# Kernel tuning notes

Measured on AMD Instinct MI355X. Metric: run time of the kernel, lower is better.

Reference implementation:

```python
import jax, jax.numpy as jnp
import numpy as np

B, S, L, E, H, T, V, D = 32, 256, 24, 300, 256, 16, 50000, 256  # batch, sents, words/sent, emb, gru_units, topics, vocab, dense


def setup_inputs() -> dict:
    key = jax.random.key(0)
    ks = jax.random.split(key, 12)
    word_ids = jax.random.randint(ks[0], (B, S, L), 0, V, dtype=jnp.int32)
    tsize = S // T
    starts = (jnp.arange(T, dtype=jnp.int32) * tsize + 1)          # 1-indexed inclusive
    ends = (jnp.arange(T, dtype=jnp.int32) * tsize + tsize)
    topic_start_ends = jnp.broadcast_to(jnp.stack([starts, ends], -1)[None], (B, T, 2))
    g = lambda k, shape, sc=0.05: (jax.random.normal(k, shape, jnp.float32) * sc)
    return {
        "word_ids": word_ids,
        "topic_start_ends": topic_start_ends,
        "emb": g(ks[1], (V, E), 0.1),
        "Wih_f": g(ks[2], (3 * H, E)), "Whh_f": g(ks[3], (3 * H, H)),
        "bih_f": jnp.zeros((3 * H,), jnp.float32), "bhh_f": jnp.zeros((3 * H,), jnp.float32),
        "Wih_b": g(ks[4], (3 * H, E)), "Whh_b": g(ks[5], (3 * H, H)),
        "bih_b": jnp.zeros((3 * H,), jnp.float32), "bhh_b": jnp.zeros((3 * H,), jnp.float32),
        "W_att": g(ks[6], (4 * H, 4 * H)), "v_att": g(ks[7], (4 * H, 1)),
        "W_dna": g(ks[8], (4 * H, D)), "b_dna": jnp.zeros((D,), jnp.float32),
        "W_out": g(ks[9], (D, 1)), "b_out": jnp.zeros((1,), jnp.float32),
    }


def _gru_dir(x, Wih, Whh, bih, bhh, reverse):
    # x: [B, S, E] -> outputs [B, S, H], final hidden [B, H]  (PyTorch GRU cell math)
    def step(h, xt):
        gi = xt @ Wih.T + bih
        gh = h @ Whh.T + bhh
        ir, iz, inn = jnp.split(gi, 3, axis=-1)
        hr, hz, hn = jnp.split(gh, 3, axis=-1)
        r = jax.nn.sigmoid(ir + hr)
        z = jax.nn.sigmoid(iz + hz)
        n = jnp.tanh(inn + r * hn)
        h2 = (1.0 - z) * n + z * h
        return h2, h2
    h0 = jnp.zeros((x.shape[0], Whh.shape[1]), x.dtype)
    hT, ys = jax.lax.scan(step, h0, jnp.swapaxes(x, 0, 1), reverse=reverse)
    return jnp.swapaxes(ys, 0, 1), hT


def _gather_seq(x, idx):
    # x: [B, S', C], idx: [B, K] -> [B, K, C]
    return jnp.take_along_axis(x, idx[:, :, None].astype(jnp.int32), axis=1)


def reference(word_ids, topic_start_ends, emb, Wih_f, Whh_f, bih_f, bhh_f,
              Wih_b, Whh_b, bih_b, bhh_b, W_att, v_att, W_dna, b_dna, W_out, b_out):
    # --- sent_encoder: per-sentence mean of word embeddings ---
    sent_vecs = jnp.mean(emb[word_ids], axis=2)  # [B, S, E]

    # --- doc_encoder: bidirectional GRU ---
    out_f, hT_f = _gru_dir(sent_vecs, Wih_f, Whh_f, bih_f, bhh_f, reverse=False)
    out_b, hT_b = _gru_dir(sent_vecs, Wih_b, Whh_b, bih_b, bhh_b, reverse=True)
    sent_rep = jnp.concatenate([out_f, out_b], axis=-1)          # [B, S, 2H]
    hidden = jnp.stack([hT_f, hT_b], axis=0)                     # [2, B, H]
    # faithful to torch: hidden.view(batch_size, 2H) (row-major reshape)
    doc_vec = hidden.reshape(B, 2 * H)
    doc_rep = jnp.broadcast_to(doc_vec[:, None, :], (B, S, 2 * H))

    # --- topic representation via boundary differencing on front/back-padded output ---
    padded = jnp.pad(sent_rep, ((0, 0), (1, 1), (0, 0)))         # [B, S+2, 2H]
    starts = topic_start_ends[..., 0]                            # [B, T], 1-indexed
    ends = topic_start_ends[..., 1]
    topic_fwd = _gather_seq(padded, ends)[..., :H] - _gather_seq(padded, starts - 1)[..., :H]
    topic_bwd = _gather_seq(padded, starts)[..., H:] - _gather_seq(padded, ends + 1)[..., H:]
    topic_mat = jnp.concatenate([topic_fwd, topic_bwd], axis=-1)  # [B, T, 2H]
    # sentence s (0-indexed) -> topic t with starts[t] <= s+1 <= ends[t]
    sent_1idx = jnp.arange(1, S + 1, dtype=jnp.int32)
    topic_id = jax.vmap(lambda e: jnp.searchsorted(e, sent_1idx, side='left'))(ends)  # [B, S]
    topic_rep = jnp.take_along_axis(topic_mat, topic_id[:, :, None], axis=1)          # [B, S, 2H]

    # --- decoder_attention ---
    cat_ds = jnp.concatenate([doc_rep, sent_rep], axis=-1)       # [B, S, 4H]
    cat_ts = jnp.concatenate([topic_rep, sent_rep], axis=-1)
    doc_scores = jnp.tanh(cat_ds @ W_att) @ v_att                # [B, S, 1]
    topic_scores = jnp.tanh(cat_ts @ W_att) @ v_att
    doc_w = jax.nn.softmax(doc_scores, axis=1)
    topic_w = jax.nn.softmax(topic_scores, axis=1)
    context = doc_w * doc_rep + topic_w * topic_rep              # [B, S, 2H]
    inp = jnp.concatenate([sent_rep, context], axis=-1)          # [B, S, 4H]
    h = jax.nn.relu(inp @ W_dna + b_dna)                         # dropout is identity (eval)
    logits = (h @ W_out + b_out)[..., 0]                         # [B, S]
    return logits
```

## Files before the change

kernel.cpp:

```cpp
#include <hip/hip_runtime.h>
#include <hip/hip_bf16.h>
#include <math.h>

#define Bd 32
#define Sd 256
#define Ld 24
#define Ed 300
#define Hd 256
#define Td 16
#define Dd 256
#define EP 320

using short8 = __attribute__((ext_vector_type(8))) short;
using f32x4  = __attribute__((ext_vector_type(4))) float;

__device__ __forceinline__ float fsigm(float x) { return 1.f / (1.f + __expf(-x)); }
__device__ __forceinline__ float ftanh(float x) {
  float e = __expf(2.f * x);
  return 1.f - 2.f / (e + 1.f);
}

__global__ void sentprep_kernel(const int* __restrict__ wids,
                                const float* __restrict__ emb,
                                __hip_bfloat16* __restrict__ apad,
                                const float* __restrict__ wih_f, const float* __restrict__ wih_b,
                                const float* __restrict__ whh_f, const float* __restrict__ whh_b,
                                __hip_bfloat16* __restrict__ wpadf, __hip_bfloat16* __restrict__ wpadb,
                                __hip_bfloat16* __restrict__ whhbf_f, __hip_bfloat16* __restrict__ whhbf_b,
                                const float* __restrict__ bih_f, const float* __restrict__ bih_b,
                                float* __restrict__ bias_cat) {
  const int blk = blockIdx.x;
  const int tid = threadIdx.x;
  if (blk < 8192) {
    __shared__ int ids[Ld];
    if (tid < Ld) ids[tid] = wids[blk * Ld + tid];
    __syncthreads();
    float acc = 0.f;
    if (tid < Ed) {
#pragma unroll
      for (int w = 0; w < Ld; ++w) acc += emb[(size_t)ids[w] * Ed + tid];
      acc *= (1.f / 24.f);
    }
    apad[blk * EP + tid] = __float2bfloat16(tid < Ed ? acc : 0.f);
    return;
  }
  const int i = (blk - 8192) * 320 + tid;
  const int PW = 768 * EP;
  const int WH = 768 * Hd;
  if (i < 2 * PW) {
    const float* src = (i < PW) ? wih_f : wih_b;
    __hip_bfloat16* dst = (i < PW) ? wpadf : wpadb;
    int j = (i < PW) ? i : i - PW;
    int n = j / EP, k = j % EP;
    dst[j] = __float2bfloat16(k < Ed ? src[n * Ed + k] : 0.f);
  } else if (i < 2 * PW + 2 * WH) {
    int j = i - 2 * PW;
    const float* src = (j < WH) ? whh_f : whh_b;
    __hip_bfloat16* dst = (j < WH) ? whhbf_f : whhbf_b;
    int k = (j < WH) ? j : j - WH;
    dst[k] = __float2bfloat16(src[k]);
  } else if (i < 2 * PW + 2 * WH + 1536) {
    int j = i - 2 * PW - 2 * WH;
    bias_cat[j] = (j < 768) ? bih_f[j] : bih_b[j - 768];
  }
}

__global__ __launch_bounds__(256) void gemm_gi_kernel(
    const __hip_bfloat16* __restrict__ A,
    const __hip_bfloat16* __restrict__ W,
    float* __restrict__ gif, float* __restrict__ gib,
    const float* __restrict__ bias_cat) {
  __shared__ unsigned short la[128][40];
  __shared__ unsigned short lb[128][40];
  const int tid = threadIdx.x;
  const int m0 = blockIdx.x * 128, n0 = blockIdx.y * 128;
  const int lane = tid & 63, wid = tid >> 6;
  const int wm = (wid >> 1) * 64, wn = (wid & 1) * 64;
  const int lrow = tid >> 2, lcol = (tid & 3) * 8;
  const int fr = lane & 15, fq = (lane >> 4) * 8;
  f32x4 acc[4][4];
#pragma unroll
  for (int i = 0; i < 4; ++i)
#pragma unroll
    for (int j = 0; j < 4; ++j) acc[i][j] = (f32x4){0.f, 0.f, 0.f, 0.f};

  for (int k0 = 0; k0 < EP; k0 += 32) {
    uint4 a0 = *(const uint4*)(A + (size_t)(m0 + lrow) * EP + k0 + lcol);
    uint4 a1 = *(const uint4*)(A + (size_t)(m0 + 64 + lrow) * EP + k0 + lcol);
    uint4 b0 = *(const uint4*)(W + (size_t)(n0 + lrow) * EP + k0 + lcol);
    uint4 b1 = *(const uint4*)(W + (size_t)(n0 + 64 + lrow) * EP + k0 + lcol);
    *(uint4*)(&la[lrow][lcol]) = a0;
    *(uint4*)(&la[64 + lrow][lcol]) = a1;
    *(uint4*)(&lb[lrow][lcol]) = b0;
    *(uint4*)(&lb[64 + lrow][lcol]) = b1;
    __syncthreads();
    short8 af[4], bf[4];
#pragma unroll
    for (int i = 0; i < 4; ++i) af[i] = *(const short8*)(&la[wm + i * 16 + fr][fq]);
#pragma unroll
    for (int j = 0; j < 4; ++j) bf[j] = *(const short8*)(&lb[wn + j * 16 + fr][fq]);
#pragma unroll
    for (int i = 0; i < 4; ++i)
#pragma unroll
      for (int j = 0; j < 4; ++j)
        acc[i][j] = __builtin_amdgcn_mfma_f32_16x16x32_bf16(af[i], bf[j], acc[i][j], 0, 0, 0);
    __syncthreads();
  }
  const int rq = (lane >> 4) * 4;
#pragma unroll
  for (int i = 0; i < 4; ++i)
#pragma unroll
    for (int j = 0; j < 4; ++j) {
      int n = n0 + wn + j * 16 + fr;
      float bv = bias_cat[n];
      float* Cp = (n < 768) ? gif : gib;
      int nn = (n < 768) ? n : n - 768;
#pragma unroll
      for (int r2 = 0; r2 < 4; ++r2) {
        int m = m0 + wm + i * 16 + rq + r2;
        Cp[(size_t)m * 768 + nn] = acc[i][j][r2] + bv;
      }
    }
}

__global__ __launch_bounds__(256) void gemm3_kernel(
    const __hip_bfloat16* __restrict__ srepbf, const __hip_bfloat16* __restrict__ topbf,
    const __hip_bfloat16* __restrict__ dvbf,
    const __hip_bfloat16* __restrict__ wpack1, const __hip_bfloat16* __restrict__ wpack2,
    float* __restrict__ QU, float* __restrict__ RT, float* __restrict__ PD) {
  const int blk = blockIdx.x;
  const __hip_bfloat16* A; const __hip_bfloat16* W; float* C;
  int M, m0, n0;
  if (blk < 640) {
    A = srepbf; W = wpack2; C = QU; M = 8192;
    m0 = (blk & 63) * 128; n0 = (blk >> 6) * 128;
  } else if (blk < 680) {
    int x = blk - 640;
    A = topbf; W = wpack1; C = RT; M = 512;
    m0 = (x & 3) * 128; n0 = (x >> 2) * 128;
  } else {
    int x = blk - 680;
    A = dvbf; W = wpack1; C = PD; M = 32;
    m0 = 0; n0 = x * 128;
  }
  __shared__ unsigned short la[128][40];
  __shared__ unsigned short lb[128][40];
  const int tid = threadIdx.x;
  const int lane = tid & 63, wid = tid >> 6;
  const int wm = (wid >> 1) * 64, wn = (wid & 1) * 64;
  const int lrow = tid >> 2, lcol = (tid & 3) * 8;
  const int fr = lane & 15, fq = (lane >> 4) * 8;
  int ar0 = m0 + lrow;      if (ar0 > M - 1) ar0 = M - 1;
  int ar1 = m0 + 64 + lrow; if (ar1 > M - 1) ar1 = M - 1;
  f32x4 acc[4][4];
#pragma unroll
  for (int i = 0; i < 4; ++i)
#pragma unroll
    for (int j = 0; j < 4; ++j) acc[i][j] = (f32x4){0.f, 0.f, 0.f, 0.f};

  for (int k0 = 0; k0 < 512; k0 += 32) {
    uint4 a0 = *(const uint4*)(A + (size_t)ar0 * 512 + k0 + lcol);
    uint4 a1 = *(const uint4*)(A + (size_t)ar1 * 512 + k0 + lcol);
    uint4 b0 = *(const uint4*)(W + (size_t)(n0 + lrow) * 512 + k0 + lcol);
    uint4 b1 = *(const uint4*)(W + (size_t)(n0 + 64 + lrow) * 512 + k0 + lcol);
    *(uint4*)(&la[lrow][lcol]) = a0;
    *(uint4*)(&la[64 + lrow][lcol]) = a1;
    *(uint4*)(&lb[lrow][lcol]) = b0;
    *(uint4*)(&lb[64 + lrow][lcol]) = b1;
    __syncthreads();
    short8 af[4], bf[4];
#pragma unroll
    for (int i = 0; i < 4; ++i) af[i] = *(const short8*)(&la[wm + i * 16 + fr][fq]);
#pragma unroll
    for (int j = 0; j < 4; ++j) bf[j] = *(const short8*)(&lb[wn + j * 16 + fr][fq]);
#pragma unroll
    for (int i = 0; i < 4; ++i)
#pragma unroll
      for (int j = 0; j < 4; ++j)
        acc[i][j] = __builtin_amdgcn_mfma_f32_16x16x32_bf16(af[i], bf[j], acc[i][j], 0, 0, 0);
    __syncthreads();
  }
  const int rq = (lane >> 4) * 4;
#pragma unroll
  for (int i = 0; i < 4; ++i)
#pragma unroll
    for (int j = 0; j < 4; ++j) {
      int n = n0 + wn + j * 16 + fr;
#pragma unroll
      for (int r2 = 0; r2 < 4; ++r2) {
        int m = m0 + wm + i * 16 + rq + r2;
        if (m < M) C[(size_t)m * 1280 + n] = acc[i][j][r2];
      }
    }
}

__global__ __launch_bounds__(512, 1) void gru_mfma_kernel(
    const float* __restrict__ gi_f, const float* __restrict__ gi_b,
    const __hip_bfloat16* __restrict__ whhbf_f, const __hip_bfloat16* __restrict__ whhbf_b,
    const float* __restrict__ bhh_f, const float* __restrict__ bhh_b,
    float* __restrict__ sent_rep, __hip_bfloat16* __restrict__ sent_rep_bf,
    float* __restrict__ hT_f, float* __restrict__ hT_b,
    const float* __restrict__ w_att, const float* __restrict__ w_dna,
    __hip_bfloat16* __restrict__ wpack1, __hip_bfloat16* __restrict__ wpack2) {
  __shared__ float gi_lds[2][8][768];
  __shared__ __hip_bfloat16 h_bf[2][256];
  __shared__ float gh[768];
  __shared__ float stg32[2][8][256];
  const int blk = blockIdx.x;
  const int tid = threadIdx.x;

  if (blk >= 64) {
    const size_t q = (size_t)(blk - 64) * 512 + tid;
    size_t flat = q * 8;
    const size_t HALF = (size_t)1280 * 512;
    const bool second = flat >= HALF;
    size_t r = second ? flat - HALF : flat;
    int n = (int)(r >> 9), k0 = (int)(r & 511);
    __hip_bfloat16* dst = second ? wpack2 : wpack1;
#pragma unroll
    for (int j = 0; j < 8; ++j) {
      int k = k0 + j;
      float v;
      if (!second)
        v = (n < 1024) ? w_att[(size_t)k * 1024 + n]
                       : w_dna[(size_t)(512 + k) * 256 + (n - 1024)];
      else
        v = (n < 1024) ? w_att[(size_t)(512 + k) * 1024 + n]
                       : w_dna[(size_t)k * 256 + (n - 1024)];
      dst[(size_t)n * 512 + k] = __float2bfloat16(v);
    }
    return;
  }

  const int dir = blk >> 5, b = blk & 31;
  const int lane = tid & 63, w = tid >> 6;
  const float* gi = dir ? gi_b : gi_f;
  const __hip_bfloat16* whh = dir ? whhbf_b : whhbf_f;
  const float* bhh = dir ? bhh_b : bhh_f;

  {
#pragma unroll
    for (int i = 0; i < 3; ++i) {
      int idx = tid + i * 512;
      int u = idx / 192;
      int c4 = (idx - u * 192) * 4;
      int s = dir ? (255 - u) : u;
      const float* g = gi + (size_t)(((b << 8) + s) * 768 + c4);
      __builtin_amdgcn_global_load_lds(
          (const __attribute__((address_space(1))) unsigned int*)g,
          (__attribute__((address_space(3))) unsigned int*)&gi_lds[0][u][c4], 16, 0, 0);
    }
  }
  if (tid < 256) h_bf[0][tid] = __float2bfloat16(0.f);

  const int fr = lane & 15, kq = (lane >> 4) * 8;
  short8 bfrag[6][8];
  {
    const int n0 = w * 96 + fr;
#pragma unroll
    for (int nt = 0; nt < 6; ++nt)
#pragma unroll
      for (int kt = 0; kt < 8; ++kt)
        bfrag[nt][kt] = *(const short8*)(whh + (size_t)(n0 + nt * 16) * 256 + kt * 32 + kq);
  }

  float bhr = 0.f, bhz = 0.f, bhn = 0.f, hprev = 0.f;
  if (tid < 256) { bhr = bhh[tid]; bhz = bhh[256 + tid]; bhn = bhh[512 + tid]; }

  asm volatile("s_waitcnt vmcnt(0) lgkmcnt(0)\n\ts_barrier" ::: "memory");

  for (int t = 0; t < Sd; ++t) {
    const int rb = t & 1, wb = rb ^ 1;

    float gl0 = 0.f, gl1 = 0.f, gl2 = 0.f;
    if (tid < 256) {
      const float* gl = gi_lds[(t >> 3) & 1][t & 7];
      gl0 = gl[tid]; gl1 = gl[256 + tid]; gl2 = gl[512 + tid];
    }

    f32x4 acc[6];
#pragma unroll
    for (int nt = 0; nt < 6; ++nt) acc[nt] = (f32x4){0.f, 0.f, 0.f, 0.f};
#pragma unroll
    for (int kt = 0; kt < 8; ++kt) {
      short8 av = *(const short8*)(&h_bf[rb][kt * 32 + kq]);
#pragma unroll
      for (int nt = 0; nt < 6; ++nt)
        acc[nt] = __builtin_amdgcn_mfma_f32_16x16x32_bf16(av, bfrag[nt][kt], acc[nt], 0, 0, 0);
      __builtin_amdgcn_sched_group_barrier(0x100, 1, 0);
      __builtin_amdgcn_sched_group_barrier(0x008, 6, 0);
    }
    if (lane < 16) {
#pragma unroll
      for (int nt = 0; nt < 6; ++nt) gh[w * 96 + nt * 16 + lane] = acc[nt][0];
    }
    asm volatile("s_waitcnt lgkmcnt(0)\n\ts_barrier" ::: "memory");

    if (tid < 256) {
      float rr = fsigm(gl0 + gh[tid] + bhr);
      float zz = fsigm(gl1 + gh[256 + tid] + bhz);
      float nn = ftanh(gl2 + rr * (gh[512 + tid] + bhn));
      float hn = (1.f - zz) * nn + zz * hprev;
      hprev = hn;
      h_bf[wb][tid] = __float2bfloat16(hn);
      stg32[(t >> 3) & 1][t & 7][tid] = hn;
    } else if ((t & 7) == 0) {
      if (t + 8 < Sd) {
        const int buf = ((t >> 3) + 1) & 1;
#pragma unroll
        for (int i = 0; i < 6; ++i) {
          int idx = (tid - 256) + i * 256;
          int u = idx / 192;
          int c4 = (idx - u * 192) * 4;
          int s = dir ? (255 - (t + 8 + u)) : (t + 8 + u);
          const float* g = gi + (size_t)(((b << 8) + s) * 768 + c4);
          __builtin_amdgcn_global_load_lds(
              (const __attribute__((address_space(1))) unsigned int*)g,
              (__attribute__((address_space(3))) unsigned int*)&gi_lds[buf][u][c4], 16, 0, 0);
        }
      }
      if (t >= 8) {
        const int base = t - 8;
        const int gp = ((t >> 3) - 1) & 1;
        const int d = tid - 256;
#pragma unroll
        for (int u = 0; u < 8; ++u) {
          int sg = dir ? (255 - (base + u)) : (base + u);
          size_t rowg = (size_t)((b << 8) + sg);
          int col = dir ? (256 + d) : d;
          float v = stg32[gp][u][d];
          sent_rep[rowg * 512 + col] = v;
          sent_rep_bf[rowg * 512 + col] = __float2bfloat16(v);
        }
      }
    }
    if (w >= 4 && (t & 7) == 7)
      asm volatile("s_waitcnt vmcnt(0)" ::: "memory");
    asm volatile("s_waitcnt lgkmcnt(0)\n\ts_barrier" ::: "memory");
  }

  if (w >= 4) {
    const int base = 248, d = tid - 256;
#pragma unroll
    for (int u = 0; u < 8; ++u) {
      int sg = dir ? (255 - (base + u)) : (base + u);
      size_t rowg = (size_t)((b << 8) + sg);
      int col = dir ? (256 + d) : d;
      float v = stg32[1][u][d];
      sent_rep[rowg * 512 + col] = v;
      sent_rep_bf[rowg * 512 + col] = __float2bfloat16(v);
    }
  } else {
    (dir ? hT_b : hT_f)[b * 256 + tid] = hprev;
  }
}

__global__ void dt_kernel(const int* __restrict__ tse, const float* __restrict__ sent_rep,
                          const float* __restrict__ hTf, const float* __restrict__ hTb,
                          __hip_bfloat16* __restrict__ topic_bf, __hip_bfloat16* __restrict__ dv) {
  const int blk = blockIdx.x;
  const int tid = threadIdx.x;
  if (blk < 512) {
    int bt = blk;
    int b = bt >> 4;
    int st = tse[bt * 2], en = tse[bt * 2 + 1];
    auto pad = [&](int i, int col) -> float {
      if (i < 1 || i > Sd) return 0.f;
      return sent_rep[((size_t)((b << 8) + (i - 1))) * 512 + col];
    };
    float fwd = pad(en, tid) - pad(st - 1, tid);
    float bwd = pad(st, Hd + tid) - pad(en + 1, Hd + tid);
    topic_bf[(size_t)bt * 512 + tid] = __float2bfloat16(fwd);
    topic_bf[(size_t)bt * 512 + Hd + tid] = __float2bfloat16(bwd);
    return;
  }
  const int b = blk - 512;
#pragma unroll
  for (int r = 0; r < 2; ++r) {
    int jj = tid + r * 256;
    int idx = b * 512 + jj;
    int dsel = idx >> 13;
    int rem = idx & 8191;
    int bp = rem >> 8, hp = rem & 255;
    float v = (dsel ? hTb : hTf)[bp * Hd + hp];
    dv[idx] = __float2bfloat16(v);
  }
}

__global__ void scores_kernel(const float* __restrict__ PD, const float* __restrict__ RT,
                              const float* __restrict__ QU, const float* __restrict__ v_att,
                              const int* __restrict__ tse,
                              float* __restrict__ dsc, float* __restrict__ tsc) {
  int r = blockIdx.x;
  int b = r >> 8, s = r & 255;
  int tid = threadIdx.x;
  int tsel = Td - 1;
  for (int t = 0; t < Td; ++t) {
    if (tse[(b * Td + t) * 2 + 1] >= s + 1) { tsel = t; break; }
  }
  const float* q = QU + (size_t)r * 1280;
  const float* p = PD + (size_t)b * 1280;
  const float* rr = RT + (size_t)(b * Td + tsel) * 1280;
  float accd = 0.f, acct = 0.f;
  for (int n = tid; n < 1024; n += 256) {
    float qv = q[n];
    float vv = v_att[n];
    accd += ftanh(p[n] + qv) * vv;
    acct += ftanh(rr[n] + qv) * vv;
  }
  __shared__ float s1[256], s2[256];
  s1[tid] = accd; s2[tid] = acct;
  __syncthreads();
  for (int off = 128; off > 0; off >>= 1) {
    if (tid < off) { s1[tid] += s1[tid + off]; s2[tid] += s2[tid + off]; }
    __syncthreads();
  }
  if (tid == 0) { dsc[r] = s1[0]; tsc[r] = s2[0]; }
}

__global__ void softmax_kernel(const float* __restrict__ dsc, const float* __restrict__ tsc,
                               float* __restrict__ dw, float* __restrict__ tw) {
  int b = blockIdx.x, s = threadIdx.x;
  __shared__ float red[256];
  for (int which = 0; which < 2; ++which) {
    const float* src = which ? tsc : dsc;
    float v = src[b * Sd + s];
    red[s] = v; __syncthreads();
    for (int off = 128; off > 0; off >>= 1) {
      if (s < off) red[s] = fmaxf(red[s], red[s + off]);
      __syncthreads();
    }
    float m = red[0]; __syncthreads();
    float e = __expf(v - m);
    red[s] = e; __syncthreads();
    for (int off = 128; off > 0; off >>= 1) {
      if (s < off) red[s] += red[s + off];
      __syncthreads();
    }
    float sum = red[0]; __syncthreads();
    (which ? tw : dw)[b * Sd + s] = e / sum;
  }
}

__global__ void final_kernel(const float* __restrict__ QU, const float* __restrict__ PD,
                             const float* __restrict__ RT, const float* __restrict__ dw,
                             const float* __restrict__ tw, const float* __restrict__ b_dna,
                             const float* __restrict__ w_out,
                             const float* __restrict__ b_out,
                             const int* __restrict__ tse, float* __restrict__ out) {
  int r = blockIdx.x;
  int b = r >> 8, s = r & 255;
  int dd = threadIdx.x;
  int tsel = Td - 1;
  for (int t = 0; t < Td; ++t) {
    if (tse[(b * Td + t) * 2 + 1] >= s + 1) { tsel = t; break; }
  }
  float wdv = dw[b * Sd + s], wtv = tw[b * Sd + s];
  float x = QU[(size_t)r * 1280 + 1024 + dd] + wdv * PD[(size_t)b * 1280 + 1024 + dd] +
            wtv * RT[(size_t)(b * Td + tsel) * 1280 + 1024 + dd] + b_dna[dd];
  x = fmaxf(x, 0.f);
  float term = x * w_out[dd];
  __shared__ float red[256];
  red[dd] = term; __syncthreads();
  for (int off = 128; off > 0; off >>= 1) {
    if (dd < off) red[dd] += red[dd + off];
    __syncthreads();
  }
  if (dd == 0) out[r] = red[0] + b_out[0];
}

extern "C" void kernel_launch(void* const* d_in, const int* in_sizes, int n_in,
                              void* d_out, int out_size, void* d_ws, size_t ws_size,
                              hipStream_t stream) {
  const int* word_ids = (const int*)d_in[0];
  const int* tse      = (const int*)d_in[1];
  const float* emb   = (const float*)d_in[2];
  const float* wih_f = (const float*)d_in[3];
  const float* whh_f = (const float*)d_in[4];
  const float* bih_f = (const float*)d_in[5];
  const float* bhh_f = (const float*)d_in[6];
  const float* wih_b = (const float*)d_in[7];
  const float* whh_b = (const float*)d_in[8];
  const float* bih_b = (const float*)d_in[9];
  const float* bhh_b = (const float*)d_in[10];
  const float* w_att = (const float*)d_in[11];
  const float* v_att = (const float*)d_in[12];
  const float* w_dna = (const float*)d_in[13];
  const float* b_dna = (const float*)d_in[14];
  const float* w_out = (const float*)d_in[15];
  const float* b_out = (const float*)d_in[16];
  float* out = (float*)d_out;
  char* ws = (char*)d_ws;

  const int M = Bd * Sd;

  size_t off = 0;
  auto alloc = [&](size_t sz) { size_t o = off; off += (sz + 255) & ~(size_t)255; return o; };
  size_t o_svbf   = alloc((size_t)M * EP * 2);
  size_t o_wpad   = alloc((size_t)2 * 768 * EP * 2);
  size_t o_whhbf  = alloc((size_t)768 * Hd * 2 * 2);
  size_t o_wpack1 = alloc((size_t)1280 * 512 * 2);
  size_t o_wpack2 = alloc((size_t)1280 * 512 * 2);
  size_t o_bcat   = alloc((size_t)1536 * 4);
  size_t o_hTf    = alloc((size_t)Bd * Hd * 4);
  size_t o_hTb    = alloc((size_t)Bd * Hd * 4);
  size_t o_dvbf   = alloc((size_t)Bd * 512 * 2);
  size_t o_topbf  = alloc((size_t)Bd * Td * 512 * 2);
  size_t o_PD     = alloc((size_t)Bd * 1280 * 4);
  size_t o_RT     = alloc((size_t)Bd * Td * 1280 * 4);
  size_t o_dsc    = alloc((size_t)Bd * Sd * 4);
  size_t o_tsc    = alloc((size_t)Bd * Sd * 4);
  size_t o_dw     = alloc((size_t)Bd * Sd * 4);
  size_t o_tw     = alloc((size_t)Bd * Sd * 4);
  size_t o_srep32 = alloc((size_t)M * 512 * 4);
  size_t o_srepbf = alloc((size_t)M * 512 * 2);
  size_t o_gif    = alloc((size_t)M * 768 * 4);
  size_t o_gib    = alloc((size_t)M * 768 * 4);
  size_t o_QU = o_gif;
  (void)ws_size;

  __hip_bfloat16* svbf   = (__hip_bfloat16*)(ws + o_svbf);
  __hip_bfloat16* wpadf  = (__hip_bfloat16*)(ws + o_wpad);
  __hip_bfloat16* wpadb  = wpadf + 768 * EP;
  __hip_bfloat16* whhbf_f = (__hip_bfloat16*)(ws + o_whhbf);
  __hip_bfloat16* whhbf_b = whhbf_f + 768 * Hd;
  __hip_bfloat16* wpack1 = (__hip_bfloat16*)(ws + o_wpack1);
  __hip_bfloat16* wpack2 = (__hip_bfloat16*)(ws + o_wpack2);
  float* bcat = (float*)(ws + o_bcat);
  float* hTf = (float*)(ws + o_hTf);
  float* hTb = (float*)(ws + o_hTb);
  __hip_bfloat16* dvbf  = (__hip_bfloat16*)(ws + o_dvbf);
  __hip_bfloat16* topbf = (__hip_bfloat16*)(ws + o_topbf);
  float* PD  = (float*)(ws + o_PD);
  float* RT  = (float*)(ws + o_RT);
  float* dsc = (float*)(ws + o_dsc);
  float* tsc = (float*)(ws + o_tsc);
  float* dw  = (float*)(ws + o_dw);
  float* tw  = (float*)(ws + o_tw);
  float* srep32 = (float*)(ws + o_srep32);
  __hip_bfloat16* srepbf = (__hip_bfloat16*)(ws + o_srepbf);
  float* gif = (float*)(ws + o_gif);
  float* gib = (float*)(ws + o_gib);
  float* QU  = (float*)(ws + o_QU);

  sentprep_kernel<<<10962, 320, 0, stream>>>(word_ids, emb, svbf,
                                             wih_f, wih_b, whh_f, whh_b,
                                             wpadf, wpadb, whhbf_f, whhbf_b,
                                             bih_f, bih_b, bcat);
  {
    dim3 grid(M / 128, 1536 / 128);
    gemm_gi_kernel<<<grid, 256, 0, stream>>>(svbf, wpadf, gif, gib, bcat);
  }
  gru_mfma_kernel<<<384, 512, 0, stream>>>(gif, gib, whhbf_f, whhbf_b, bhh_f, bhh_b,
                                           srep32, srepbf, hTf, hTb,
                                           w_att, w_dna, wpack1, wpack2);
  dt_kernel<<<544, 256, 0, stream>>>(tse, srep32, hTf, hTb, topbf, dvbf);
  gemm3_kernel<<<690, 256, 0, stream>>>(srepbf, topbf, dvbf, wpack1, wpack2, QU, RT, PD);
  scores_kernel<<<M, 256, 0, stream>>>(PD, RT, QU, v_att, tse, dsc, tsc);
  softmax_kernel<<<Bd, 256, 0, stream>>>(dsc, tsc, dw, tw);
  final_kernel<<<M, 256, 0, stream>>>(QU, PD, RT, dw, tw, b_dna, w_out, b_out, tse, out);
}
```

Measured before the change: 536.7 us.

## Fuse post-GRU kernels using atomic counters and flag spin-waits

Merges the topic/doc-vector prep with the three projection GEMMs into one launch. The GEMM blocks that need the prep outputs spin on a global flag set by the last prep block. It also merges scores, softmax and the final dense into one per-row kernel, where the last block of each batch computes the softmax and publishes a flag that the other blocks spin on. This removes three kernel launches and their drain gaps, but the spin-waits assume the producer blocks get scheduled. With 8192 blocks in the attention kernel, forward progress depends on dispatch order, so it could hang or stall.

```diff
diff --git a/kernel.cpp b/kernel.cpp
--- a/kernel.cpp
+++ b/kernel.cpp
@@ -20,6 +20,8 @@
   return 1.f - 2.f / (e + 1.f);
 }
 
+#define SYNC_N 66
+
 __global__ void sentprep_kernel(const int* __restrict__ wids,
                                 const float* __restrict__ emb,
                                 __hip_bfloat16* __restrict__ apad,
@@ -28,7 +30,8 @@
                                 __hip_bfloat16* __restrict__ wpadf, __hip_bfloat16* __restrict__ wpadb,
                                 __hip_bfloat16* __restrict__ whhbf_f, __hip_bfloat16* __restrict__ whhbf_b,
                                 const float* __restrict__ bih_f, const float* __restrict__ bih_b,
-                                float* __restrict__ bias_cat) {
+                                float* __restrict__ bias_cat,
+                                int* __restrict__ syncbuf) {
   const int blk = blockIdx.x;
   const int tid = threadIdx.x;
   if (blk < 8192) {
@@ -47,6 +50,7 @@
   const int i = (blk - 8192) * 320 + tid;
   const int PW = 768 * EP;
   const int WH = 768 * Hd;
+  const int SYNC0 = 2 * PW + 2 * WH + 1536;
   if (i < 2 * PW) {
     const float* src = (i < PW) ? wih_f : wih_b;
     __hip_bfloat16* dst = (i < PW) ? wpadf : wpadb;
@@ -59,9 +63,11 @@
     __hip_bfloat16* dst = (j < WH) ? whhbf_f : whhbf_b;
     int k = (j < WH) ? j : j - WH;
     dst[k] = __float2bfloat16(src[k]);
-  } else if (i < 2 * PW + 2 * WH + 1536) {
+  } else if (i < SYNC0) {
     int j = i - 2 * PW - 2 * WH;
     bias_cat[j] = (j < 768) ? bih_f[j] : bih_b[j - 768];
+  } else if (i < SYNC0 + SYNC_N) {
+    syncbuf[i - SYNC0] = 0;
   }
 }
 
@@ -119,77 +125,6 @@
       for (int r2 = 0; r2 < 4; ++r2) {
         int m = m0 + wm + i * 16 + rq + r2;
         Cp[(size_t)m * 768 + nn] = acc[i][j][r2] + bv;
-      }
-    }
-}
-
-__global__ __launch_bounds__(256) void gemm3_kernel(
-    const __hip_bfloat16* __restrict__ srepbf, const __hip_bfloat16* __restrict__ topbf,
-    const __hip_bfloat16* __restrict__ dvbf,
-    const __hip_bfloat16* __restrict__ wpack1, const __hip_bfloat16* __restrict__ wpack2,
-    float* __restrict__ QU, float* __restrict__ RT, float* __restrict__ PD) {
-  const int blk = blockIdx.x;
-  const __hip_bfloat16* A; const __hip_bfloat16* W; float* C;
-  int M, m0, n0;
-  if (blk < 640) {
-    A = srepbf; W = wpack2; C = QU; M = 8192;
-    m0 = (blk & 63) * 128; n0 = (blk >> 6) * 128;
-  } else if (blk < 680) {
-    int x = blk - 640;
-    A = topbf; W = wpack1; C = RT; M = 512;
-    m0 = (x & 3) * 128; n0 = (x >> 2) * 128;
-  } else {
-    int x = blk - 680;
-    A = dvbf; W = wpack1; C = PD; M = 32;
-    m0 = 0; n0 = x * 128;
-  }
-  __shared__ unsigned short la[128][40];
-  __shared__ unsigned short lb[128][40];
-  const int tid = threadIdx.x;
-  const int lane = tid & 63, wid = tid >> 6;
-  const int wm = (wid >> 1) * 64, wn = (wid & 1) * 64;
-  const int lrow = tid >> 2, lcol = (tid & 3) * 8;
-  const int fr = lane & 15, fq = (lane >> 4) * 8;
-  int ar0 = m0 + lrow;      if (ar0 > M - 1) ar0 = M - 1;
-  int ar1 = m0 + 64 + lrow; if (ar1 > M - 1) ar1 = M - 1;
-  f32x4 acc[4][4];
-#pragma unroll
-  for (int i = 0; i < 4; ++i)
-#pragma unroll
-    for (int j = 0; j < 4; ++j) acc[i][j] = (f32x4){0.f, 0.f, 0.f, 0.f};
-
-  for (int k0 = 0; k0 < 512; k0 += 32) {
-    uint4 a0 = *(const uint4*)(A + (size_t)ar0 * 512 + k0 + lcol);
-    uint4 a1 = *(const uint4*)(A + (size_t)ar1 * 512 + k0 + lcol);
-    uint4 b0 = *(const uint4*)(W + (size_t)(n0 + lrow) * 512 + k0 + lcol);
-    uint4 b1 = *(const uint4*)(W + (size_t)(n0 + 64 + lrow) * 512 + k0 + lcol);
-    *(uint4*)(&la[lrow][lcol]) = a0;
-    *(uint4*)(&la[64 + lrow][lcol]) = a1;
-    *(uint4*)(&lb[lrow][lcol]) = b0;
-    *(uint4*)(&lb[64 + lrow][lcol]) = b1;
-    __syncthreads();
-    short8 af[4], bf[4];
-#pragma unroll
-    for (int i = 0; i < 4; ++i) af[i] = *(const short8*)(&la[wm + i * 16 + fr][fq]);
-#pragma unroll
-    for (int j = 0; j < 4; ++j) bf[j] = *(const short8*)(&lb[wn + j * 16 + fr][fq]);
-#pragma unroll
-    for (int i = 0; i < 4; ++i)
-#pragma unroll
-      for (int j = 0; j < 4; ++j)
-        acc[i][j] = __builtin_amdgcn_mfma_f32_16x16x32_bf16(af[i], bf[j], acc[i][j], 0, 0, 0);
-    __syncthreads();
-  }
-  const int rq = (lane >> 4) * 4;
-#pragma unroll
-  for (int i = 0; i < 4; ++i)
-#pragma unroll
-    for (int j = 0; j < 4; ++j) {
-      int n = n0 + wn + j * 16 + fr;
-#pragma unroll
-      for (int r2 = 0; r2 < 4; ++r2) {
-        int m = m0 + wm + i * 16 + rq + r2;
-        if (m < M) C[(size_t)m * 1280 + n] = acc[i][j][r2];
       }
     }
 }
@@ -355,45 +290,138 @@
   }
 }
 
-__global__ void dt_kernel(const int* __restrict__ tse, const float* __restrict__ sent_rep,
-                          const float* __restrict__ hTf, const float* __restrict__ hTb,
-                          __hip_bfloat16* __restrict__ topic_bf, __hip_bfloat16* __restrict__ dv) {
+__global__ __launch_bounds__(256) void dtgemm3_kernel(
+    const int* __restrict__ tse, const float* __restrict__ sent_rep,
+    const float* __restrict__ hTf, const float* __restrict__ hTb,
+    __hip_bfloat16* __restrict__ topic_bf, __hip_bfloat16* __restrict__ dv,
+    const __hip_bfloat16* __restrict__ srepbf,
+    const __hip_bfloat16* __restrict__ wpack1, const __hip_bfloat16* __restrict__ wpack2,
+    float* __restrict__ QU, float* __restrict__ RT, float* __restrict__ PD,
+    int* __restrict__ cnt2, int* __restrict__ flag2) {
   const int blk = blockIdx.x;
   const int tid = threadIdx.x;
-  if (blk < 512) {
-    int bt = blk;
-    int b = bt >> 4;
-    int st = tse[bt * 2], en = tse[bt * 2 + 1];
-    auto pad = [&](int i, int col) -> float {
-      if (i < 1 || i > Sd) return 0.f;
-      return sent_rep[((size_t)((b << 8) + (i - 1))) * 512 + col];
-    };
-    float fwd = pad(en, tid) - pad(st - 1, tid);
-    float bwd = pad(st, Hd + tid) - pad(en + 1, Hd + tid);
-    topic_bf[(size_t)bt * 512 + tid] = __float2bfloat16(fwd);
-    topic_bf[(size_t)bt * 512 + Hd + tid] = __float2bfloat16(bwd);
+  __shared__ unsigned short la[128][40];
+  __shared__ unsigned short lb[128][40];
+
+  if (blk < 544) {
+    if (blk < 512) {
+      int bt = blk;
+      int b = bt >> 4;
+      int st = tse[bt * 2], en = tse[bt * 2 + 1];
+      auto pad = [&](int i, int col) -> float {
+        if (i < 1 || i > Sd) return 0.f;
+        return sent_rep[((size_t)((b << 8) + (i - 1))) * 512 + col];
+      };
+      float fwd = pad(en, tid) - pad(st - 1, tid);
+      float bwd = pad(st, Hd + tid) - pad(en + 1, Hd + tid);
+      topic_bf[(size_t)bt * 512 + tid] = __float2bfloat16(fwd);
+      topic_bf[(size_t)bt * 512 + Hd + tid] = __float2bfloat16(bwd);
+    } else {
+      const int b = blk - 512;
+#pragma unroll
+      for (int r = 0; r < 2; ++r) {
+        int jj = tid + r * 256;
+        int idx = b * 512 + jj;
+        int dsel = idx >> 13;
+        int rem = idx & 8191;
+        int bp = rem >> 8, hp = rem & 255;
+        float v = (dsel ? hTb : hTf)[bp * Hd + hp];
+        dv[idx] = __float2bfloat16(v);
+      }
+    }
+    __threadfence();
+    __syncthreads();
+    if (tid == 0) {
+      if (atomicAdd(cnt2, 1) == 543)
+        __hip_atomic_store(flag2, 1, __ATOMIC_RELEASE, __HIP_MEMORY_SCOPE_AGENT);
+    }
     return;
   }
-  const int b = blk - 512;
-#pragma unroll
-  for (int r = 0; r < 2; ++r) {
-    int jj = tid + r * 256;
-    int idx = b * 512 + jj;
-    int dsel = idx >> 13;
-    int rem = idx & 8191;
-    int bp = rem >> 8, hp = rem & 255;
-    float v = (dsel ? hTb : hTf)[bp * Hd + hp];
-    dv[idx] = __float2bfloat16(v);
-  }
-}
-
-__global__ void scores_kernel(const float* __restrict__ PD, const float* __restrict__ RT,
-                              const float* __restrict__ QU, const float* __restrict__ v_att,
-                              const int* __restrict__ tse,
-                              float* __restrict__ dsc, float* __restrict__ tsc) {
-  int r = blockIdx.x;
-  int b = r >> 8, s = r & 255;
-  int tid = threadIdx.x;
+
+  const int g = blk - 544;
+  const __hip_bfloat16* A; const __hip_bfloat16* W; float* C;
+  int M, m0, n0;
+  if (g < 640) {
+    A = srepbf; W = wpack2; C = QU; M = 8192;
+    m0 = (g & 63) * 128; n0 = (g >> 6) * 128;
+  } else if (g < 680) {
+    int x = g - 640;
+    A = topic_bf; W = wpack1; C = RT; M = 512;
+    m0 = (x & 3) * 128; n0 = (x >> 2) * 128;
+  } else {
+    int x = g - 680;
+    A = dv; W = wpack1; C = PD; M = 32;
+    m0 = 0; n0 = x * 128;
+  }
+  if (g >= 640) {
+    if (tid == 0) {
+      while (__hip_atomic_load(flag2, __ATOMIC_ACQUIRE, __HIP_MEMORY_SCOPE_AGENT) == 0)
+        __builtin_amdgcn_s_sleep(8);
+    }
+    __syncthreads();
+  }
+
+  const int lane = tid & 63, wid = tid >> 6;
+  const int wm = (wid >> 1) * 64, wn = (wid & 1) * 64;
+  const int lrow = tid >> 2, lcol = (tid & 3) * 8;
+  const int fr = lane & 15, fq = (lane >> 4) * 8;
+  int ar0 = m0 + lrow;      if (ar0 > M - 1) ar0 = M - 1;
+  int ar1 = m0 + 64 + lrow; if (ar1 > M - 1) ar1 = M - 1;
+  f32x4 acc[4][4];
+#pragma unroll
+  for (int i = 0; i < 4; ++i)
+#pragma unroll
+    for (int j = 0; j < 4; ++j) acc[i][j] = (f32x4){0.f, 0.f, 0.f, 0.f};
+
+  for (int k0 = 0; k0 < 512; k0 += 32) {
+    uint4 a0 = *(const uint4*)(A + (size_t)ar0 * 512 + k0 + lcol);
+    uint4 a1 = *(const uint4*)(A + (size_t)ar1 * 512 + k0 + lcol);
+    uint4 b0 = *(const uint4*)(W + (size_t)(n0 + lrow) * 512 + k0 + lcol);
+    uint4 b1 = *(const uint4*)(W + (size_t)(n0 + 64 + lrow) * 512 + k0 + lcol);
+    *(uint4*)(&la[lrow][lcol]) = a0;
+    *(uint4*)(&la[64 + lrow][lcol]) = a1;
+    *(uint4*)(&lb[lrow][lcol]) = b0;
+    *(uint4*)(&lb[64 + lrow][lcol]) = b1;
+    __syncthreads();
+    short8 af[4], bf[4];
+#pragma unroll
+    for (int i = 0; i < 4; ++i) af[i] = *(const short8*)(&la[wm + i * 16 + fr][fq]);
+#pragma unroll
+    for (int j = 0; j < 4; ++j) bf[j] = *(const short8*)(&lb[wn + j * 16 + fr][fq]);
+#pragma unroll
+    for (int i = 0; i < 4; ++i)
+#pragma unroll
+      for (int j = 0; j < 4; ++j)
+        acc[i][j] = __builtin_amdgcn_mfma_f32_16x16x32_bf16(af[i], bf[j], acc[i][j], 0, 0, 0);
+    __syncthreads();
+  }
+  const int rq = (lane >> 4) * 4;
+#pragma unroll
+  for (int i = 0; i < 4; ++i)
+#pragma unroll
+    for (int j = 0; j < 4; ++j) {
+      int n = n0 + wn + j * 16 + fr;
+#pragma unroll
+      for (int r2 = 0; r2 < 4; ++r2) {
+        int m = m0 + wm + i * 16 + rq + r2;
+        if (m < M) C[(size_t)m * 1280 + n] = acc[i][j][r2];
+      }
+    }
+}
+
+__global__ __launch_bounds__(256) void attn_kernel(
+    const float* __restrict__ PD, const float* __restrict__ RT,
+    const float* __restrict__ QU, const float* __restrict__ v_att,
+    const int* __restrict__ tse,
+    const float* __restrict__ b_dna, const float* __restrict__ w_out,
+    const float* __restrict__ b_out,
+    float* __restrict__ dsc, float* __restrict__ tsc,
+    float* __restrict__ dw, float* __restrict__ tw,
+    int* __restrict__ cnt, int* __restrict__ flag,
+    float* __restrict__ out) {
+  const int r = blockIdx.x, b = r >> 8, s = r & 255, tid = threadIdx.x;
+  __shared__ float s1[256], s2[256];
+  __shared__ int amlast;
   int tsel = Td - 1;
   for (int t = 0; t < Td; ++t) {
     if (tse[(b * Td + t) * 2 + 1] >= s + 1) { tsel = t; break; }
@@ -408,65 +436,64 @@
     accd += ftanh(p[n] + qv) * vv;
     acct += ftanh(rr[n] + qv) * vv;
   }
-  __shared__ float s1[256], s2[256];
   s1[tid] = accd; s2[tid] = acct;
   __syncthreads();
   for (int off = 128; off > 0; off >>= 1) {
     if (tid < off) { s1[tid] += s1[tid + off]; s2[tid] += s2[tid + off]; }
     __syncthreads();
   }
-  if (tid == 0) { dsc[r] = s1[0]; tsc[r] = s2[0]; }
-}
-
-__global__ void softmax_kernel(const float* __restrict__ dsc, const float* __restrict__ tsc,
-                               float* __restrict__ dw, float* __restrict__ tw) {
-  int b = blockIdx.x, s = threadIdx.x;
-  __shared__ float red[256];
-  for (int which = 0; which < 2; ++which) {
-    const float* src = which ? tsc : dsc;
-    float v = src[b * Sd + s];
-    red[s] = v; __syncthreads();
+  if (tid == 0) {
+    dsc[r] = s1[0]; tsc[r] = s2[0];
+    __threadfence();
+    amlast = (atomicAdd(&cnt[b], 1) == 255) ? 1 : 0;
+  }
+  __syncthreads();
+
+  if (amlast) {
+    float v1 = dsc[b * 256 + tid], v2 = tsc[b * 256 + tid];
+    s1[tid] = v1; s2[tid] = v2;
+    __syncthreads();
     for (int off = 128; off > 0; off >>= 1) {
-      if (s < off) red[s] = fmaxf(red[s], red[s + off]);
+      if (tid < off) {
+        s1[tid] = fmaxf(s1[tid], s1[tid + off]);
+        s2[tid] = fmaxf(s2[tid], s2[tid + off]);
+      }
       __syncthreads();
     }
-    float m = red[0]; __syncthreads();
-    float e = __expf(v - m);
-    red[s] = e; __syncthreads();
+    float m1 = s1[0], m2 = s2[0];
+    __syncthreads();
+    float e1 = __expf(v1 - m1), e2 = __expf(v2 - m2);
+    s1[tid] = e1; s2[tid] = e2;
+    __syncthreads();
     for (int off = 128; off > 0; off >>= 1) {
-      if (s < off) red[s] += red[s + off];
+      if (tid < off) { s1[tid] += s1[tid + off]; s2[tid] += s2[tid + off]; }
       __syncthreads();
     }
-    float sum = red[0]; __syncthreads();
-    (which ? tw : dw)[b * Sd + s] = e / sum;
-  }
-}
-
-__global__ void final_kernel(const float* __restrict__ QU, const float* __restrict__ PD,
-                             const float* __restrict__ RT, const float* __restrict__ dw,
-                             const float* __restrict__ tw, const float* __restrict__ b_dna,
-                             const float* __restrict__ w_out,
-                             const float* __restrict__ b_out,
-                             const int* __restrict__ tse, float* __restrict__ out) {
-  int r = blockIdx.x;
-  int b = r >> 8, s = r & 255;
-  int dd = threadIdx.x;
-  int tsel = Td - 1;
-  for (int t = 0; t < Td; ++t) {
-    if (tse[(b * Td + t) * 2 + 1] >= s + 1) { tsel = t; break; }
-  }
-  float wdv = dw[b * Sd + s], wtv = tw[b * Sd + s];
-  float x = QU[(size_t)r * 1280 + 1024 + dd] + wdv * PD[(size_t)b * 1280 + 1024 + dd] +
-            wtv * RT[(size_t)(b * Td + tsel) * 1280 + 1024 + dd] + b_dna[dd];
+    dw[b * 256 + tid] = e1 / s1[0];
+    tw[b * 256 + tid] = e2 / s2[0];
+    __threadfence();
+    __syncthreads();
+    if (tid == 0)
+      __hip_atomic_store(&flag[b], 1, __ATOMIC_RELEASE, __HIP_MEMORY_SCOPE_AGENT);
+  }
+
+  if (tid == 0) {
+    while (__hip_atomic_load(&flag[b], __ATOMIC_ACQUIRE, __HIP_MEMORY_SCOPE_AGENT) == 0)
+      __builtin_amdgcn_s_sleep(8);
+  }
+  __syncthreads();
+
+  float wdv = dw[b * 256 + s], wtv = tw[b * 256 + s];
+  float x = QU[(size_t)r * 1280 + 1024 + tid] + wdv * PD[(size_t)b * 1280 + 1024 + tid] +
+            wtv * RT[(size_t)(b * Td + tsel) * 1280 + 1024 + tid] + b_dna[tid];
   x = fmaxf(x, 0.f);
-  float term = x * w_out[dd];
-  __shared__ float red[256];
-  red[dd] = term; __syncthreads();
+  s1[tid] = x * w_out[tid];
+  __syncthreads();
   for (int off = 128; off > 0; off >>= 1) {
-    if (dd < off) red[dd] += red[dd + off];
-    __syncthreads();
-  }
-  if (dd == 0) out[r] = red[0] + b_out[0];
+    if (tid < off) s1[tid] += s1[tid + off];
+    __syncthreads();
+  }
+  if (tid == 0) out[r] = s1[0] + b_out[0];
 }
 
 extern "C" void kernel_launch(void* const* d_in, const int* in_sizes, int n_in,
@@ -502,6 +529,7 @@
   size_t o_wpack1 = alloc((size_t)1280 * 512 * 2);
   size_t o_wpack2 = alloc((size_t)1280 * 512 * 2);
   size_t o_bcat   = alloc((size_t)1536 * 4);
+  size_t o_sync   = alloc((size_t)SYNC_N * 4);
   size_t o_hTf    = alloc((size_t)Bd * Hd * 4);
   size_t o_hTb    = alloc((size_t)Bd * Hd * 4);
   size_t o_dvbf   = alloc((size_t)Bd * 512 * 2);
@@ -521,12 +549,12 @@
 
   __hip_bfloat16* svbf   = (__hip_bfloat16*)(ws + o_svbf);
   __hip_bfloat16* wpadf  = (__hip_bfloat16*)(ws + o_wpad);
-  __hip_bfloat16* wpadb  = wpadf + 768 * EP;
   __hip_bfloat16* whhbf_f = (__hip_bfloat16*)(ws + o_whhbf);
   __hip_bfloat16* whhbf_b = whhbf_f + 768 * Hd;
   __hip_bfloat16* wpack1 = (__hip_bfloat16*)(ws + o_wpack1);
   __hip_bfloat16* wpack2 = (__hip_bfloat16*)(ws + o_wpack2);
   float* bcat = (float*)(ws + o_bcat);
+  int* syncbuf = (int*)(ws + o_sync);
   float* hTf = (float*)(ws + o_hTf);
   float* hTb = (float*)(ws + o_hTb);
   __hip_bfloat16* dvbf  = (__hip_bfloat16*)(ws + o_dvbf);
@@ -545,8 +573,8 @@
 
   sentprep_kernel<<<10962, 320, 0, stream>>>(word_ids, emb, svbf,
                                              wih_f, wih_b, whh_f, whh_b,
-                                             wpadf, wpadb, whhbf_f, whhbf_b,
-                                             bih_f, bih_b, bcat);
+                                             wpadf, wpadf + 768 * EP, whhbf_f, whhbf_b,
+                                             bih_f, bih_b, bcat, syncbuf);
   {
     dim3 grid(M / 128, 1536 / 128);
     gemm_gi_kernel<<<grid, 256, 0, stream>>>(svbf, wpadf, gif, gib, bcat);
@@ -554,9 +582,9 @@
   gru_mfma_kernel<<<384, 512, 0, stream>>>(gif, gib, whhbf_f, whhbf_b, bhh_f, bhh_b,
                                            srep32, srepbf, hTf, hTb,
                                            w_att, w_dna, wpack1, wpack2);
-  dt_kernel<<<544, 256, 0, stream>>>(tse, srep32, hTf, hTb, topbf, dvbf);
-  gemm3_kernel<<<690, 256, 0, stream>>>(srepbf, topbf, dvbf, wpack1, wpack2, QU, RT, PD);
-  scores_kernel<<<M, 256, 0, stream>>>(PD, RT, QU, v_att, tse, dsc, tsc);
-  softmax_kernel<<<Bd, 256, 0, stream>>>(dsc, tsc, dw, tw);
-  final_kernel<<<M, 256, 0, stream>>>(QU, PD, RT, dw, tw, b_dna, w_out, b_out, tse, out);
-}
+  dtgemm3_kernel<<<1234, 256, 0, stream>>>(tse, srep32, hTf, hTb, topbf, dvbf,
+                                           srepbf, wpack1, wpack2, QU, RT, PD,
+                                           syncbuf + 64, syncbuf + 65);
+  attn_kernel<<<M, 256, 0, stream>>>(PD, RT, QU, v_att, tse, b_dna, w_out, b_out,
+                                     dsc, tsc, dw, tw, syncbuf, syncbuf + 32, out);
+}
```

Result: slower. 1.108 ms (+106.5%).
